# Optimization experiments

Measured on AMD Instinct MI355X. Metric: run time of the kernel, lower is better.

Reference implementation:

```python
import jax, jax.numpy as jnp
import numpy as np

N_RES = 131072
MSA_C = 384
HID = 128
N_BLOCK = 2
N_RESTYPE = 21


def l2_normalize(x, eps=1e-12):
    s = jnp.sum(x.astype(jnp.float32) ** 2, axis=-1, keepdims=True)
    return (x / jnp.sqrt(jnp.maximum(s, eps))).astype(x.dtype)


def quat_to_rot(q):
    q = q / jnp.sqrt(jnp.maximum(jnp.sum(q * q, axis=-1, keepdims=True), 1e-12))
    w, x, y, z = q[..., 0], q[..., 1], q[..., 2], q[..., 3]
    r00 = 1 - 2 * (y * y + z * z); r01 = 2 * (x * y - w * z); r02 = 2 * (x * z + w * y)
    r10 = 2 * (x * y + w * z); r11 = 1 - 2 * (x * x + z * z); r12 = 2 * (y * z - w * x)
    r20 = 2 * (x * z - w * y); r21 = 2 * (y * z + w * x); r22 = 1 - 2 * (x * x + y * y)
    return jnp.stack([jnp.stack([r00, r01, r02], -1),
                      jnp.stack([r10, r11, r12], -1),
                      jnp.stack([r20, r21, r22], -1)], axis=-2)


def setup_inputs() -> dict:
    key = jax.random.key(0)
    ks = jax.random.split(key, 20)
    d = {}
    d['affine'] = jax.random.normal(ks[0], (N_RES, 7), jnp.float32)
    d['rep0'] = jax.random.normal(ks[1], (N_RES, MSA_C), jnp.float32)
    d['rep1'] = jax.random.normal(ks[2], (N_RES, MSA_C), jnp.float32)
    d['aatype'] = jax.random.randint(ks[3], (N_RES,), 0, N_RESTYPE, jnp.int32)
    sc = 0.05
    d['w_in0'] = jax.random.normal(ks[4], (MSA_C, HID), jnp.float32) * sc
    d['b_in0'] = jnp.zeros((HID,), jnp.float32)
    d['w_in1'] = jax.random.normal(ks[5], (MSA_C, HID), jnp.float32) * sc
    d['b_in1'] = jnp.zeros((HID,), jnp.float32)
    d['Wr1'] = jax.random.normal(ks[6], (N_BLOCK, HID, HID), jnp.float32) * sc
    d['br1'] = jnp.zeros((N_BLOCK, HID), jnp.float32)
    d['Wr2'] = jax.random.normal(ks[7], (N_BLOCK, HID, HID), jnp.float32) * sc
    d['br2'] = jnp.zeros((N_BLOCK, HID), jnp.float32)
    d['w_ang'] = jax.random.normal(ks[8], (HID, 14), jnp.float32) * sc
    d['b_ang'] = jnp.zeros((14,), jnp.float32)
    # literature geometry tables (AF2 shapes; random stand-ins for correctness baseline)
    d['default_frames'] = jax.random.normal(ks[9], (N_RESTYPE, 8, 4, 4), jnp.float32)
    d['group_idx'] = jax.random.randint(ks[10], (N_RESTYPE, 14), 0, 8, jnp.int32)
    d['atom_mask'] = (jax.random.uniform(ks[11], (N_RESTYPE, 14)) > 0.2).astype(jnp.float32)
    d['lit_positions'] = jax.random.normal(ks[12], (N_RESTYPE, 14, 3), jnp.float32)
    return d


def reference(affine, rep0, rep1, aatype, w_in0, b_in0, w_in1, b_in1, Wr1, br1,
              Wr2, br2, w_ang, b_ang, default_frames, group_idx, atom_mask, lit_positions):
    # MLP trunk
    act = (jax.nn.relu(rep0) @ w_in0 + b_in0) + (jax.nn.relu(rep1) @ w_in1 + b_in1)
    for i in range(Wr1.shape[0]):
        old = act
        act = jax.nn.relu(act) @ Wr1[i] + br1[i]
        act = jax.nn.relu(act) @ Wr2[i] + br2[i]
        act = act + old
    n = act.shape[0]
    unnorm = (jax.nn.relu(act) @ w_ang + b_ang).reshape(n, 7, 2)
    angles = l2_normalize(unnorm)

    # backbone rigid from quat-affine
    rot_b = quat_to_rot(affine[:, :4])          # [N,3,3]
    trans_b = affine[:, 4:]                     # [N,3]

    # torsion_angles_to_frames
    sin = jnp.concatenate([jnp.zeros((n, 1), angles.dtype), angles[..., 0]], axis=-1)  # [N,8]
    cos = jnp.concatenate([jnp.ones((n, 1), angles.dtype), angles[..., 1]], axis=-1)
    z = jnp.zeros_like(sin); o = jnp.ones_like(sin)
    all_rots = jnp.stack([jnp.stack([o, z, z], -1),
                          jnp.stack([z, cos, -sin], -1),
                          jnp.stack([z, sin, cos], -1)], axis=-2)     # [N,8,3,3]
    m = default_frames[aatype]                   # [N,8,4,4] gather
    rot_f = jnp.einsum('ngij,ngjk->ngik', m[..., :3, :3], all_rots)   # [N,8,3,3]
    trans_f = m[..., :3, 3]                      # [N,8,3]

    def compose(r1, t1, r2, t2):
        return jnp.einsum('nij,njk->nik', r1, r2), jnp.einsum('nij,nj->ni', r1, t2) + t1

    r5, t5 = compose(rot_f[:, 4], trans_f[:, 4], rot_f[:, 5], trans_f[:, 5])  # chi2->backb
    r6, t6 = compose(r5, t5, rot_f[:, 6], trans_f[:, 6])                       # chi3->backb
    r7, t7 = compose(r6, t6, rot_f[:, 7], trans_f[:, 7])                       # chi4->backb
    rot_all = jnp.concatenate([rot_f[:, :5], jnp.stack([r5, r6, r7], 1)], axis=1)    # [N,8,3,3]
    trans_all = jnp.concatenate([trans_f[:, :5], jnp.stack([t5, t6, t7], 1)], axis=1)

    rot_g = jnp.einsum('nij,ngjk->ngik', rot_b, rot_all)                # [N,8,3,3]
    trans_g = jnp.einsum('nij,ngj->ngi', rot_b, trans_all) + trans_b[:, None]

    # frames_and_literature_positions_to_atom14_pos
    gm = jax.nn.one_hot(group_idx[aatype], 8, dtype=rot_g.dtype)        # [N,14,8]
    rot_a = jnp.einsum('nag,ngij->naij', gm, rot_g)                     # [N,14,3,3]
    trans_a = jnp.einsum('nag,ngi->nai', gm, trans_g)                   # [N,14,3]
    lit = lit_positions[aatype]                                         # [N,14,3]
    pos = jnp.einsum('naij,naj->nai', rot_a, lit) + trans_a
    pos = pos * atom_mask[aatype][..., None]
    return angles, unnorm, pos, rot_g, trans_g
```

## Files before the change

kernel.cpp:

```cpp
#include <hip/hip_runtime.h>
#include <stdint.h>

typedef _Float16 f16x8 __attribute__((ext_vector_type(8)));
typedef float floatx4 __attribute__((ext_vector_type(4)));

__device__ __forceinline__ void f2h2(float x, unsigned short& hi, unsigned short& lo) {
  _Float16 h = (_Float16)x;
  float r = (x - (float)h) * 2048.0f;
  _Float16 l = (_Float16)r;
  union { _Float16 f; unsigned short u; } a, b;
  a.f = h; b.f = l;
  hi = a.u; lo = b.u;
}

__global__ __launch_bounds__(256) void k0_convert(
    const float* __restrict__ w_in0, const float* __restrict__ w_in1,
    const float* __restrict__ Wr1, const float* __restrict__ Wr2,
    const float* __restrict__ w_ang,
    unsigned short* __restrict__ btH, unsigned short* __restrict__ btL,
    unsigned short* __restrict__ wrtH, unsigned short* __restrict__ wrtL,
    unsigned short* __restrict__ angtH, unsigned short* __restrict__ angtL) {
  int e = blockIdx.x * 256 + threadIdx.x;
  if (e < 128 * 768) {
    int n = e / 768, k = e % 768;
    float v = (k < 384) ? w_in0[k * 128 + n] : w_in1[(k - 384) * 128 + n];
    f2h2(v, btH[e], btL[e]);
  }
  if (e < 4 * 128 * 128) {
    int mi = e / 16384, rem = e % 16384;
    int n = rem / 128, k = rem % 128;
    int blk = mi >> 1, which = mi & 1;
    const float* W = which ? Wr2 : Wr1;
    f2h2(W[blk * 16384 + k * 128 + n], wrtH[e], wrtL[e]);
  }
  if (e < 16 * 128) {
    int n = e / 128, k = e % 128;
    float v = (n < 14) ? w_ang[k * 14 + n] : 0.0f;
    f2h2(v, angtH[e], angtL[e]);
  }
}

__global__ __launch_bounds__(256) void k1_gemm_in(
    const float* __restrict__ rep0, const float* __restrict__ rep1,
    const float* __restrict__ b_in0, const float* __restrict__ b_in1,
    const unsigned short* __restrict__ btH, const unsigned short* __restrict__ btL,
    float* __restrict__ act) {
  __shared__ unsigned short AbH[128 * 40], AbL[128 * 40];
  __shared__ unsigned short BbH[128 * 40], BbL[128 * 40];
  const int tid = threadIdx.x;
  const int lane = tid & 63, w = tid >> 6;
  const int q = lane >> 4, m = lane & 15;
  const int row0 = blockIdx.x * 128;

  floatx4 acc1[2][8], acc2[2][8];
#pragma unroll
  for (int rt = 0; rt < 2; ++rt)
#pragma unroll
    for (int ct = 0; ct < 8; ++ct) {
      acc1[rt][ct] = (floatx4){0.f, 0.f, 0.f, 0.f};
      acc2[rt][ct] = (floatx4){0.f, 0.f, 0.f, 0.f};
    }

  for (int s = 0; s < 24; ++s) {
    __syncthreads();
    const float* __restrict__ rep = (s < 12) ? rep0 : rep1;
    const int cb = (s < 12 ? s : s - 12) * 32;
#pragma unroll
    for (int r = 0; r < 4; ++r) {
      int f4 = tid + 256 * r;
      int row = f4 >> 3, k4 = (f4 & 7) << 2;
      float4 v = *reinterpret_cast<const float4*>(
          rep + (size_t)(row0 + row) * 384 + cb + k4);
      unsigned short h0, h1, h2, h3, l0, l1, l2, l3;
      f2h2(fmaxf(v.x, 0.f), h0, l0);
      f2h2(fmaxf(v.y, 0.f), h1, l1);
      f2h2(fmaxf(v.z, 0.f), h2, l2);
      f2h2(fmaxf(v.w, 0.f), h3, l3);
      uint2 ph, pl;
      ph.x = h0 | ((unsigned)h1 << 16); ph.y = h2 | ((unsigned)h3 << 16);
      pl.x = l0 | ((unsigned)l1 << 16); pl.y = l2 | ((unsigned)l3 << 16);
      *reinterpret_cast<uint2*>(&AbH[row * 40 + k4]) = ph;
      *reinterpret_cast<uint2*>(&AbL[row * 40 + k4]) = pl;
    }
#pragma unroll
    for (int r = 0; r < 2; ++r) {
      int c = tid + 256 * r;
      int nr = c >> 2, k8 = (c & 3) << 3;
      *reinterpret_cast<uint4*>(&BbH[nr * 40 + k8]) =
          *reinterpret_cast<const uint4*>(btH + nr * 768 + s * 32 + k8);
      *reinterpret_cast<uint4*>(&BbL[nr * 40 + k8]) =
          *reinterpret_cast<const uint4*>(btL + nr * 768 + s * 32 + k8);
    }
    __syncthreads();
    f16x8 ah[2], al[2];
#pragma unroll
    for (int rt = 0; rt < 2; ++rt) {
      ah[rt] = *reinterpret_cast<const f16x8*>(&AbH[(w * 32 + rt * 16 + m) * 40 + q * 8]);
      al[rt] = *reinterpret_cast<const f16x8*>(&AbL[(w * 32 + rt * 16 + m) * 40 + q * 8]);
    }
#pragma unroll
    for (int ct = 0; ct < 8; ++ct) {
      f16x8 bh = *reinterpret_cast<const f16x8*>(&BbH[(ct * 16 + m) * 40 + q * 8]);
      f16x8 bl = *reinterpret_cast<const f16x8*>(&BbL[(ct * 16 + m) * 40 + q * 8]);
#pragma unroll
      for (int rt = 0; rt < 2; ++rt) {
        acc1[rt][ct] = __builtin_amdgcn_mfma_f32_16x16x32_f16(ah[rt], bh, acc1[rt][ct], 0, 0, 0);
        acc2[rt][ct] = __builtin_amdgcn_mfma_f32_16x16x32_f16(ah[rt], bl, acc2[rt][ct], 0, 0, 0);
        acc2[rt][ct] = __builtin_amdgcn_mfma_f32_16x16x32_f16(al[rt], bh, acc2[rt][ct], 0, 0, 0);
      }
    }
  }
  const float S = 1.0f / 2048.0f;
#pragma unroll
  for (int rt = 0; rt < 2; ++rt)
#pragma unroll
    for (int ct = 0; ct < 8; ++ct) {
      int col = ct * 16 + m;
      float bias = b_in0[col] + b_in1[col];
#pragma unroll
      for (int reg = 0; reg < 4; ++reg) {
        int row = row0 + w * 32 + rt * 16 + q * 4 + reg;
        act[(size_t)row * 128 + col] = acc1[rt][ct][reg] + acc2[rt][ct][reg] * S + bias;
      }
    }
}

__global__ __launch_bounds__(256) void k2_resnet(
    const float* __restrict__ act,
    const unsigned short* __restrict__ wrtH, const unsigned short* __restrict__ wrtL,
    const float* __restrict__ br1, const float* __restrict__ br2,
    const unsigned short* __restrict__ angtH, const unsigned short* __restrict__ angtL,
    const float* __restrict__ b_ang, float* __restrict__ out_unnorm) {
  __shared__ unsigned short XbH[128 * 136], XbL[128 * 136];
  __shared__ unsigned short WbH[128 * 40], WbL[128 * 40];
  const int tid = threadIdx.x;
  const int lane = tid & 63, w = tid >> 6;
  const int q = lane >> 4, m = lane & 15;
  const int row0 = blockIdx.x * 128;
  const float S = 1.0f / 2048.0f;

  floatx4 cur[2][8];
#pragma unroll
  for (int rt = 0; rt < 2; ++rt)
#pragma unroll
    for (int ct = 0; ct < 8; ++ct) {
      int col = ct * 16 + m;
#pragma unroll
      for (int reg = 0; reg < 4; ++reg) {
        int rl = w * 32 + rt * 16 + q * 4 + reg;
        float v = act[(size_t)(row0 + rl) * 128 + col];
        cur[rt][ct][reg] = v;
        f2h2(fmaxf(v, 0.f), XbH[rl * 136 + col], XbL[rl * 136 + col]);
      }
    }

  auto gemm = [&](const unsigned short* __restrict__ WH,
                  const unsigned short* __restrict__ WL,
                  floatx4 a1[2][8], floatx4 a2[2][8]) {
    for (int s = 0; s < 4; ++s) {
      __syncthreads();
#pragma unroll
      for (int r = 0; r < 2; ++r) {
        int c = tid + 256 * r;
        int nr = c >> 2, k8 = (c & 3) << 3;
        *reinterpret_cast<uint4*>(&WbH[nr * 40 + k8]) =
            *reinterpret_cast<const uint4*>(WH + nr * 128 + s * 32 + k8);
        *reinterpret_cast<uint4*>(&WbL[nr * 40 + k8]) =
            *reinterpret_cast<const uint4*>(WL + nr * 128 + s * 32 + k8);
      }
      __syncthreads();
      f16x8 ah[2], al[2];
#pragma unroll
      for (int rt = 0; rt < 2; ++rt) {
        ah[rt] = *reinterpret_cast<const f16x8*>(&XbH[(w * 32 + rt * 16 + m) * 136 + s * 32 + q * 8]);
        al[rt] = *reinterpret_cast<const f16x8*>(&XbL[(w * 32 + rt * 16 + m) * 136 + s * 32 + q * 8]);
      }
#pragma unroll
      for (int ct = 0; ct < 8; ++ct) {
        f16x8 bh = *reinterpret_cast<const f16x8*>(&WbH[(ct * 16 + m) * 40 + q * 8]);
        f16x8 bl = *reinterpret_cast<const f16x8*>(&WbL[(ct * 16 + m) * 40 + q * 8]);
#pragma unroll
        for (int rt = 0; rt < 2; ++rt) {
          a1[rt][ct] = __builtin_amdgcn_mfma_f32_16x16x32_f16(ah[rt], bh, a1[rt][ct], 0, 0, 0);
          a2[rt][ct] = __builtin_amdgcn_mfma_f32_16x16x32_f16(ah[rt], bl, a2[rt][ct], 0, 0, 0);
          a2[rt][ct] = __builtin_amdgcn_mfma_f32_16x16x32_f16(al[rt], bh, a2[rt][ct], 0, 0, 0);
        }
      }
    }
  };

  for (int i = 0; i < 2; ++i) {
    floatx4 a1[2][8], a2[2][8];
#pragma unroll
    for (int rt = 0; rt < 2; ++rt)
#pragma unroll
      for (int ct = 0; ct < 8; ++ct) {
        a1[rt][ct] = (floatx4){0.f, 0.f, 0.f, 0.f};
        a2[rt][ct] = (floatx4){0.f, 0.f, 0.f, 0.f};
      }
    gemm(wrtH + (size_t)(i * 2 + 0) * 16384, wrtL + (size_t)(i * 2 + 0) * 16384, a1, a2);
    __syncthreads();
#pragma unroll
    for (int rt = 0; rt < 2; ++rt)
#pragma unroll
      for (int ct = 0; ct < 8; ++ct) {
        int col = ct * 16 + m;
        float b = br1[i * 128 + col];
#pragma unroll
        for (int reg = 0; reg < 4; ++reg) {
          int rl = w * 32 + rt * 16 + q * 4 + reg;
          float v = a1[rt][ct][reg] + a2[rt][ct][reg] * S + b;
          f2h2(fmaxf(v, 0.f), XbH[rl * 136 + col], XbL[rl * 136 + col]);
        }
      }
    floatx4 c1[2][8], c2[2][8];
#pragma unroll
    for (int rt = 0; rt < 2; ++rt)
#pragma unroll
      for (int ct = 0; ct < 8; ++ct) {
        c1[rt][ct] = cur[rt][ct];
        c2[rt][ct] = (floatx4){0.f, 0.f, 0.f, 0.f};
      }
    gemm(wrtH + (size_t)(i * 2 + 1) * 16384, wrtL + (size_t)(i * 2 + 1) * 16384, c1, c2);
    __syncthreads();
#pragma unroll
    for (int rt = 0; rt < 2; ++rt)
#pragma unroll
      for (int ct = 0; ct < 8; ++ct) {
        int col = ct * 16 + m;
        float b = br2[i * 128 + col];
#pragma unroll
        for (int reg = 0; reg < 4; ++reg) {
          int rl = w * 32 + rt * 16 + q * 4 + reg;
          float v = c1[rt][ct][reg] + c2[rt][ct][reg] * S + b;
          cur[rt][ct][reg] = v;
          f2h2(fmaxf(v, 0.f), XbH[rl * 136 + col], XbL[rl * 136 + col]);
        }
      }
  }

  floatx4 A1[2], A2[2];
  A1[0] = (floatx4){0.f, 0.f, 0.f, 0.f}; A1[1] = A1[0];
  A2[0] = A1[0]; A2[1] = A1[0];
  for (int s = 0; s < 4; ++s) {
    __syncthreads();
    if (tid < 64) {
      int nr = tid >> 2, k8 = (tid & 3) << 3;
      *reinterpret_cast<uint4*>(&WbH[nr * 40 + k8]) =
          *reinterpret_cast<const uint4*>(angtH + nr * 128 + s * 32 + k8);
      *reinterpret_cast<uint4*>(&WbL[nr * 40 + k8]) =
          *reinterpret_cast<const uint4*>(angtL + nr * 128 + s * 32 + k8);
    }
    __syncthreads();
    f16x8 bh = *reinterpret_cast<const f16x8*>(&WbH[m * 40 + q * 8]);
    f16x8 bl = *reinterpret_cast<const f16x8*>(&WbL[m * 40 + q * 8]);
#pragma unroll
    for (int rt = 0; rt < 2; ++rt) {
      f16x8 ah = *reinterpret_cast<const f16x8*>(&XbH[(w * 32 + rt * 16 + m) * 136 + s * 32 + q * 8]);
      f16x8 al = *reinterpret_cast<const f16x8*>(&XbL[(w * 32 + rt * 16 + m) * 136 + s * 32 + q * 8]);
      A1[rt] = __builtin_amdgcn_mfma_f32_16x16x32_f16(ah, bh, A1[rt], 0, 0, 0);
      A2[rt] = __builtin_amdgcn_mfma_f32_16x16x32_f16(ah, bl, A2[rt], 0, 0, 0);
      A2[rt] = __builtin_amdgcn_mfma_f32_16x16x32_f16(al, bh, A2[rt], 0, 0, 0);
    }
  }
  if (m < 14) {
    float bias = b_ang[m];
#pragma unroll
    for (int rt = 0; rt < 2; ++rt)
#pragma unroll
      for (int reg = 0; reg < 4; ++reg) {
        int row = row0 + w * 32 + rt * 16 + q * 4 + reg;
        out_unnorm[(size_t)row * 14 + m] = A1[rt][reg] + A2[rt][reg] * S + bias;
      }
  }
}

__global__ __launch_bounds__(64) void k3_geom(
    const float* __restrict__ affine, const int* __restrict__ aatype,
    const float* __restrict__ dframes, const int* __restrict__ gidx,
    const float* __restrict__ amask, const float* __restrict__ lpos,
    float* __restrict__ out, int n) {
  __shared__ float lds[96 * 64];
  const int tid = threadIdx.x;
  const int r = blockIdx.x * 64 + tid;
  const size_t OFF0 = 0;
  const size_t OFF1 = (size_t)n * 14;
  const size_t OFF2 = (size_t)n * 28;
  const size_t OFF3 = (size_t)n * 70;
  const size_t OFF4 = (size_t)n * 142;

  float ang[14];
  const float* un = out + OFF1 + (size_t)r * 14;
#pragma unroll
  for (int j = 0; j < 7; ++j) {
    float a = un[2 * j], b = un[2 * j + 1];
    float inv = 1.0f / sqrtf(fmaxf(a * a + b * b, 1e-12f));
    ang[2 * j] = a * inv;
    ang[2 * j + 1] = b * inv;
    out[OFF0 + (size_t)r * 14 + 2 * j] = ang[2 * j];
    out[OFF0 + (size_t)r * 14 + 2 * j + 1] = ang[2 * j + 1];
  }

  const float* af = affine + (size_t)r * 7;
  float qw = af[0], qx = af[1], qy = af[2], qz = af[3];
  float qi = 1.0f / sqrtf(fmaxf(qw * qw + qx * qx + qy * qy + qz * qz, 1e-12f));
  qw *= qi; qx *= qi; qy *= qi; qz *= qi;
  float rb[9];
  rb[0] = 1.f - 2.f * (qy * qy + qz * qz);
  rb[1] = 2.f * (qx * qy - qw * qz);
  rb[2] = 2.f * (qx * qz + qw * qy);
  rb[3] = 2.f * (qx * qy + qw * qz);
  rb[4] = 1.f - 2.f * (qx * qx + qz * qz);
  rb[5] = 2.f * (qy * qz - qw * qx);
  rb[6] = 2.f * (qx * qz - qw * qy);
  rb[7] = 2.f * (qy * qz + qw * qx);
  rb[8] = 1.f - 2.f * (qx * qx + qy * qy);
  float tb0 = af[4], tb1 = af[5], tb2 = af[6];

  int aat = aatype[r];
  const float* mb = dframes + (size_t)aat * 128;
  float sa[8], ca[8];
  sa[0] = 0.f; ca[0] = 1.f;
#pragma unroll
  for (int g = 1; g < 8; ++g) { sa[g] = ang[(g - 1) * 2]; ca[g] = ang[(g - 1) * 2 + 1]; }

  float chr[9], cht[3];
#pragma unroll
  for (int g = 0; g < 8; ++g) {
    const float* M = mb + g * 16;
    float c = ca[g], s = sa[g];
    float rf[9], tf[3];
#pragma unroll
    for (int i = 0; i < 3; ++i) {
      float m1 = M[i * 4 + 1], m2 = M[i * 4 + 2];
      rf[i * 3 + 0] = M[i * 4 + 0];
      rf[i * 3 + 1] = m1 * c + m2 * s;
      rf[i * 3 + 2] = m2 * c - m1 * s;
      tf[i] = M[i * 4 + 3];
    }
    float ra[9], ta[3];
    if (g < 5) {
#pragma unroll
      for (int e = 0; e < 9; ++e) ra[e] = rf[e];
      ta[0] = tf[0]; ta[1] = tf[1]; ta[2] = tf[2];
      if (g == 4) {
#pragma unroll
        for (int e = 0; e < 9; ++e) chr[e] = rf[e];
        cht[0] = tf[0]; cht[1] = tf[1]; cht[2] = tf[2];
      }
    } else {
      float nr[9], nt[3];
#pragma unroll
      for (int i = 0; i < 3; ++i) {
#pragma unroll
        for (int j = 0; j < 3; ++j)
          nr[i * 3 + j] = chr[i * 3 + 0] * rf[0 + j] + chr[i * 3 + 1] * rf[3 + j] +
                          chr[i * 3 + 2] * rf[6 + j];
        nt[i] = chr[i * 3 + 0] * tf[0] + chr[i * 3 + 1] * tf[1] +
                chr[i * 3 + 2] * tf[2] + cht[i];
      }
#pragma unroll
      for (int e = 0; e < 9; ++e) { chr[e] = nr[e]; ra[e] = nr[e]; }
      cht[0] = nt[0]; cht[1] = nt[1]; cht[2] = nt[2];
      ta[0] = nt[0]; ta[1] = nt[1]; ta[2] = nt[2];
    }
    float rg[9], tg[3];
#pragma unroll
    for (int i = 0; i < 3; ++i) {
#pragma unroll
      for (int j = 0; j < 3; ++j)
        rg[i * 3 + j] = rb[i * 3 + 0] * ra[0 + j] + rb[i * 3 + 1] * ra[3 + j] +
                        rb[i * 3 + 2] * ra[6 + j];
      tg[i] = rb[i * 3 + 0] * ta[0] + rb[i * 3 + 1] * ta[1] + rb[i * 3 + 2] * ta[2];
    }
    tg[0] += tb0; tg[1] += tb1; tg[2] += tb2;
#pragma unroll
    for (int e = 0; e < 9; ++e) {
      out[OFF3 + (size_t)r * 72 + g * 9 + e] = rg[e];
      lds[(g * 12 + e) * 64 + tid] = rg[e];
    }
#pragma unroll
    for (int i = 0; i < 3; ++i) {
      out[OFF4 + (size_t)r * 24 + g * 3 + i] = tg[i];
      lds[(g * 12 + 9 + i) * 64 + tid] = tg[i];
    }
  }

#pragma unroll
  for (int a = 0; a < 14; ++a) {
    int gi = gidx[aat * 14 + a];
    float mask = amask[aat * 14 + a];
    const float* lp = lpos + (size_t)(aat * 14 + a) * 3;
    float l0 = lp[0], l1 = lp[1], l2 = lp[2];
    int b = gi * 12;
#pragma unroll
    for (int i = 0; i < 3; ++i) {
      float p = lds[(b + i * 3 + 0) * 64 + tid] * l0 +
                lds[(b + i * 3 + 1) * 64 + tid] * l1 +
                lds[(b + i * 3 + 2) * 64 + tid] * l2 + lds[(b + 9 + i) * 64 + tid];
      out[OFF2 + (size_t)r * 42 + a * 3 + i] = p * mask;
    }
  }
}

extern "C" void kernel_launch(void* const* d_in, const int* in_sizes, int n_in,
                              void* d_out, int out_size, void* d_ws, size_t ws_size,
                              hipStream_t stream) {
  const float* affine = (const float*)d_in[0];
  const float* rep0 = (const float*)d_in[1];
  const float* rep1 = (const float*)d_in[2];
  const int* aatype = (const int*)d_in[3];
  const float* w_in0 = (const float*)d_in[4];
  const float* b_in0 = (const float*)d_in[5];
  const float* w_in1 = (const float*)d_in[6];
  const float* b_in1 = (const float*)d_in[7];
  const float* Wr1 = (const float*)d_in[8];
  const float* br1 = (const float*)d_in[9];
  const float* Wr2 = (const float*)d_in[10];
  const float* br2 = (const float*)d_in[11];
  const float* w_ang = (const float*)d_in[12];
  const float* b_ang = (const float*)d_in[13];
  const float* dframes = (const float*)d_in[14];
  const int* gidx = (const int*)d_in[15];
  const float* amask = (const float*)d_in[16];
  const float* lpos = (const float*)d_in[17];
  float* out = (float*)d_out;

  const int n = in_sizes[0] / 7;

  char* ws = (char*)d_ws;
  unsigned short* btH = (unsigned short*)ws;
  unsigned short* btL = btH + 98304;
  unsigned short* wrtH = btL + 98304;
  unsigned short* wrtL = wrtH + 65536;
  unsigned short* angtH = wrtL + 65536;
  unsigned short* angtL = angtH + 2048;
  size_t w_bytes = (size_t)(2 * (98304 + 65536 + 2048)) * sizeof(unsigned short);
  size_t act_off = (w_bytes + 255) & ~(size_t)255;
  float* act;
  if (ws_size >= act_off + (size_t)n * 128 * sizeof(float)) {
    act = (float*)(ws + act_off);
  } else {
    act = out + (size_t)n * 28;
  }

  k0_convert<<<384, 256, 0, stream>>>(w_in0, w_in1, Wr1, Wr2, w_ang,
                                      btH, btL, wrtH, wrtL, angtH, angtL);
  k1_gemm_in<<<n / 128, 256, 0, stream>>>(rep0, rep1, b_in0, b_in1, btH, btL, act);
  k2_resnet<<<n / 128, 256, 0, stream>>>(act, wrtH, wrtL, br1, br2, angtH, angtL,
                                         b_ang, out + (size_t)n * 14);
  k3_geom<<<n / 64, 64, 0, stream>>>(affine, aatype, dframes, gidx, amask, lpos,
                                     out, n);
}
```

Measured before the change: 680.3 us.

## Double-buffer input GEMM with async global-to-LDS loads and fragment-native layouts

Rewrites the input-projection GEMM to prefetch the next K-slice of rep and the split-f16 weights straight into double-buffered LDS using global_load_lds, with vmcnt waits and raw barriers. The fp32-to-hi/lo f16 split moves from the staging phase to register time, just before the MFMAs. The weights are pre-permuted into MFMA-fragment order, and the intermediate activation buffer is stored in a per-wave fragment layout so both the GEMM epilogue and the resnet kernel read and write it as contiguous float4. The aim is to overlap global-memory latency with compute and to remove scattered scalar stores, in exchange for more conversion work per MFMA tile and hand-tuned wait counts.

```diff
diff --git a/kernel.cpp b/kernel.cpp
--- a/kernel.cpp
+++ b/kernel.cpp
@@ -11,6 +11,12 @@
   union { _Float16 f; unsigned short u; } a, b;
   a.f = h; b.f = l;
   hi = a.u; lo = b.u;
+}
+
+__device__ __forceinline__ void async_copy16(void* lds, const void* gsrc) {
+  __builtin_amdgcn_global_load_lds(
+      (const __attribute__((address_space(1))) unsigned int*)gsrc,
+      (__attribute__((address_space(3))) unsigned int*)lds, 16, 0, 0);
 }
 
 __global__ __launch_bounds__(256) void k0_convert(
@@ -21,8 +27,11 @@
     unsigned short* __restrict__ wrtH, unsigned short* __restrict__ wrtL,
     unsigned short* __restrict__ angtH, unsigned short* __restrict__ angtL) {
   int e = blockIdx.x * 256 + threadIdx.x;
-  if (e < 128 * 768) {
-    int n = e / 768, k = e % 768;
+  if (e < 24 * 4096) {
+    int s = e >> 12, rem = e & 4095;
+    int ct = rem >> 9, lane = (rem >> 3) & 63, el = rem & 7;
+    int n = ct * 16 + (lane & 15);
+    int k = s * 32 + ((lane >> 4) << 3) + el;
     float v = (k < 384) ? w_in0[k * 128 + n] : w_in1[(k - 384) * 128 + n];
     f2h2(v, btH[e], btL[e]);
   }
@@ -45,12 +54,22 @@
     const float* __restrict__ b_in0, const float* __restrict__ b_in1,
     const unsigned short* __restrict__ btH, const unsigned short* __restrict__ btL,
     float* __restrict__ act) {
-  __shared__ unsigned short AbH[128 * 40], AbL[128 * 40];
-  __shared__ unsigned short BbH[128 * 40], BbL[128 * 40];
+  __shared__ float Ab[2][4096];
+  __shared__ unsigned short BH[2][4096];
+  __shared__ unsigned short BL[2][4096];
   const int tid = threadIdx.x;
   const int lane = tid & 63, w = tid >> 6;
-  const int q = lane >> 4, m = lane & 15;
+  const int m = lane & 15;
   const int row0 = blockIdx.x * 128;
+
+  int aoff[4], adst[4];
+#pragma unroll
+  for (int r = 0; r < 4; ++r) {
+    int rp = r & 1, h = r >> 1;
+    aoff[r] = (row0 + (w * 2 + rp) * 16 + m) * 384 + ((lane >> 4) << 3) + h * 4;
+    adst[r] = h * 2048 + (w * 2 + rp) * 256;
+  }
+  const int bsrc0 = (w * 2) * 512 + lane * 8;
 
   floatx4 acc1[2][8], acc2[2][8];
 #pragma unroll
@@ -61,47 +80,51 @@
       acc2[rt][ct] = (floatx4){0.f, 0.f, 0.f, 0.f};
     }
 
-  for (int s = 0; s < 24; ++s) {
-    __syncthreads();
+  auto stage = [&](int pb, int s) {
     const float* __restrict__ rep = (s < 12) ? rep0 : rep1;
     const int cb = (s < 12 ? s : s - 12) * 32;
 #pragma unroll
-    for (int r = 0; r < 4; ++r) {
-      int f4 = tid + 256 * r;
-      int row = f4 >> 3, k4 = (f4 & 7) << 2;
-      float4 v = *reinterpret_cast<const float4*>(
-          rep + (size_t)(row0 + row) * 384 + cb + k4);
-      unsigned short h0, h1, h2, h3, l0, l1, l2, l3;
-      f2h2(fmaxf(v.x, 0.f), h0, l0);
-      f2h2(fmaxf(v.y, 0.f), h1, l1);
-      f2h2(fmaxf(v.z, 0.f), h2, l2);
-      f2h2(fmaxf(v.w, 0.f), h3, l3);
-      uint2 ph, pl;
-      ph.x = h0 | ((unsigned)h1 << 16); ph.y = h2 | ((unsigned)h3 << 16);
-      pl.x = l0 | ((unsigned)l1 << 16); pl.y = l2 | ((unsigned)l3 << 16);
-      *reinterpret_cast<uint2*>(&AbH[row * 40 + k4]) = ph;
-      *reinterpret_cast<uint2*>(&AbL[row * 40 + k4]) = pl;
-    }
+    for (int r = 0; r < 4; ++r)
+      async_copy16(&Ab[pb][adst[r]], rep + aoff[r] + cb);
 #pragma unroll
     for (int r = 0; r < 2; ++r) {
-      int c = tid + 256 * r;
-      int nr = c >> 2, k8 = (c & 3) << 3;
-      *reinterpret_cast<uint4*>(&BbH[nr * 40 + k8]) =
-          *reinterpret_cast<const uint4*>(btH + nr * 768 + s * 32 + k8);
-      *reinterpret_cast<uint4*>(&BbL[nr * 40 + k8]) =
-          *reinterpret_cast<const uint4*>(btL + nr * 768 + s * 32 + k8);
-    }
-    __syncthreads();
+      async_copy16(&BH[pb][(w * 2 + r) * 512], btH + (size_t)s * 4096 + bsrc0 + r * 512);
+      async_copy16(&BL[pb][(w * 2 + r) * 512], btL + (size_t)s * 4096 + bsrc0 + r * 512);
+    }
+  };
+
+  stage(0, 0);
+#pragma unroll 2
+  for (int s = 0; s < 24; ++s) {
+    const int pb = s & 1;
+    if (s < 23) {
+      stage(pb ^ 1, s + 1);
+      asm volatile("s_waitcnt vmcnt(8)" ::: "memory");
+    } else {
+      asm volatile("s_waitcnt vmcnt(0)" ::: "memory");
+    }
+    __builtin_amdgcn_s_barrier();
+    asm volatile("" ::: "memory");
+
     f16x8 ah[2], al[2];
 #pragma unroll
     for (int rt = 0; rt < 2; ++rt) {
-      ah[rt] = *reinterpret_cast<const f16x8*>(&AbH[(w * 32 + rt * 16 + m) * 40 + q * 8]);
-      al[rt] = *reinterpret_cast<const f16x8*>(&AbL[(w * 32 + rt * 16 + m) * 40 + q * 8]);
+      const float* ap = &Ab[pb][((w * 2 + rt) * 64 + lane) * 4];
+      float4 x0 = *reinterpret_cast<const float4*>(ap);
+      float4 x1 = *reinterpret_cast<const float4*>(ap + 2048);
+      float xs[8] = {x0.x, x0.y, x0.z, x0.w, x1.x, x1.y, x1.z, x1.w};
+#pragma unroll
+      for (int e = 0; e < 8; ++e) {
+        float x = fmaxf(xs[e], 0.f);
+        _Float16 hh = (_Float16)x;
+        ah[rt][e] = hh;
+        al[rt][e] = (_Float16)((x - (float)hh) * 2048.0f);
+      }
     }
 #pragma unroll
     for (int ct = 0; ct < 8; ++ct) {
-      f16x8 bh = *reinterpret_cast<const f16x8*>(&BbH[(ct * 16 + m) * 40 + q * 8]);
-      f16x8 bl = *reinterpret_cast<const f16x8*>(&BbL[(ct * 16 + m) * 40 + q * 8]);
+      f16x8 bh = *reinterpret_cast<const f16x8*>(&BH[pb][(ct * 64 + lane) * 8]);
+      f16x8 bl = *reinterpret_cast<const f16x8*>(&BL[pb][(ct * 64 + lane) * 8]);
 #pragma unroll
       for (int rt = 0; rt < 2; ++rt) {
         acc1[rt][ct] = __builtin_amdgcn_mfma_f32_16x16x32_f16(ah[rt], bh, acc1[rt][ct], 0, 0, 0);
@@ -109,19 +132,24 @@
         acc2[rt][ct] = __builtin_amdgcn_mfma_f32_16x16x32_f16(al[rt], bh, acc2[rt][ct], 0, 0, 0);
       }
     }
-  }
+    asm volatile("" ::: "memory");
+    __builtin_amdgcn_s_barrier();
+    asm volatile("" ::: "memory");
+  }
+
   const float S = 1.0f / 2048.0f;
+  float* aout = act + ((size_t)blockIdx.x * 4 + w) * 4096 + (size_t)lane * 4;
 #pragma unroll
   for (int rt = 0; rt < 2; ++rt)
 #pragma unroll
     for (int ct = 0; ct < 8; ++ct) {
       int col = ct * 16 + m;
       float bias = b_in0[col] + b_in1[col];
-#pragma unroll
-      for (int reg = 0; reg < 4; ++reg) {
-        int row = row0 + w * 32 + rt * 16 + q * 4 + reg;
-        act[(size_t)row * 128 + col] = acc1[rt][ct][reg] + acc2[rt][ct][reg] * S + bias;
-      }
+      floatx4 v;
+#pragma unroll
+      for (int reg = 0; reg < 4; ++reg)
+        v[reg] = acc1[rt][ct][reg] + acc2[rt][ct][reg] * S + bias;
+      *reinterpret_cast<floatx4*>(aout + (rt * 8 + ct) * 256) = v;
     }
 }
 
@@ -140,17 +168,18 @@
   const float S = 1.0f / 2048.0f;
 
   floatx4 cur[2][8];
+  const float* ain = act + ((size_t)blockIdx.x * 4 + w) * 4096 + (size_t)lane * 4;
 #pragma unroll
   for (int rt = 0; rt < 2; ++rt)
 #pragma unroll
     for (int ct = 0; ct < 8; ++ct) {
+      floatx4 v = *reinterpret_cast<const floatx4*>(ain + (rt * 8 + ct) * 256);
+      cur[rt][ct] = v;
       int col = ct * 16 + m;
 #pragma unroll
       for (int reg = 0; reg < 4; ++reg) {
         int rl = w * 32 + rt * 16 + q * 4 + reg;
-        float v = act[(size_t)(row0 + rl) * 128 + col];
-        cur[rt][ct][reg] = v;
-        f2h2(fmaxf(v, 0.f), XbH[rl * 136 + col], XbL[rl * 136 + col]);
+        f2h2(fmaxf(v[reg], 0.f), XbH[rl * 136 + col], XbL[rl * 136 + col]);
       }
     }
 
```

After: 676.3 us. Within noise of the previous version (-0.6%).
